# Optimization experiments

Measured on AMD Instinct MI355X. Metric: run time of the kernel, lower is better.

The kernel has to match this reference:

```python
import jax, jax.numpy as jnp
import numpy as np

SCALE = 8.0  # sqrt(d_k), d_k = 64


def setup_inputs() -> dict:
    key = jax.random.key(0)
    kq, kk, kv = jax.random.split(key, 3)
    B, S, D = 16, 2048, 64
    q = jax.random.normal(kq, (B, S, D), dtype=jnp.float32)
    k = jax.random.normal(kk, (B, S, D), dtype=jnp.float32)
    v = jax.random.normal(kv, (B, S, D), dtype=jnp.float32)
    # causal mask: True = masked (future positions), broadcast to batch
    causal = jnp.triu(jnp.ones((S, S), dtype=jnp.bool_), k=1)
    mask = jnp.broadcast_to(causal, (B, S, S))
    return {"q": q, "k": k, "v": v, "mask": mask}


def reference(q, k, v, mask):
    # u = (q @ k^T) / scale  -> [B, S, S]
    u = jnp.einsum("bqd,bkd->bqk", q, k) / SCALE
    u = jnp.where(mask, -jnp.inf, u)
    attn = jax.nn.softmax(u, axis=2)
    output = jnp.einsum("bqk,bkd->bqd", attn, v)
    return (attn, output)
```

## Files before the change

kernel.cpp:

```cpp
#include <hip/hip_runtime.h>
#include <hip/hip_bf16.h>

typedef __attribute__((ext_vector_type(4))) float  f32x4;
typedef __attribute__((ext_vector_type(8))) __bf16 bf16x8;
typedef __attribute__((ext_vector_type(4))) __bf16 bf16x4;

#define S_DIM 2048
#define D_DIM 64
#define A2    0.180336880f
#define TPITCH 68

__device__ __forceinline__ int swz(int r, int c) {
    return r * 64 + (c ^ ((r & 7) << 3));
}

__device__ __forceinline__ void loadK4(const float* Kb, int kt, int tid, f32x4 kr[4]) {
    #pragma unroll
    for (int i = 0; i < 4; ++i)
        kr[i] = *(const f32x4*)(Kb + (size_t)(kt * 64 + (tid >> 4) + i * 16) * D_DIM
                                + (tid & 15) * 4);
}
__device__ __forceinline__ void writeK4(__bf16* buf, int tid, const f32x4 kr[4]) {
    #pragma unroll
    for (int i = 0; i < 4; ++i) {
        bf16x4 h;
        h[0] = (__bf16)kr[i][0]; h[1] = (__bf16)kr[i][1];
        h[2] = (__bf16)kr[i][2]; h[3] = (__bf16)kr[i][3];
        *(bf16x4*)&buf[swz((tid >> 4) + i * 16, (tid & 15) * 4)] = h;
    }
}
__device__ __forceinline__ void loadQfrag(const float* Qb, int w, int c0, int jb, bf16x8 qf[2]) {
    const float* qp = Qb + (w * 16 + c0) * D_DIM + jb * 8;
    #pragma unroll
    for (int h = 0; h < 2; ++h) {
        f32x4 x0 = *(const f32x4*)(qp + h * 32);
        f32x4 x1 = *(const f32x4*)(qp + h * 32 + 4);
        bf16x8 f;
        f[0] = (__bf16)x0[0]; f[1] = (__bf16)x0[1];
        f[2] = (__bf16)x0[2]; f[3] = (__bf16)x0[3];
        f[4] = (__bf16)x1[0]; f[5] = (__bf16)x1[1];
        f[6] = (__bf16)x1[2]; f[7] = (__bf16)x1[3];
        qf[h] = f;
    }
}
__device__ __forceinline__ void mfmaS(const __bf16* bufK, const bf16x8 qf[2],
                                      int c0, int jb, f32x4 sacc[4]) {
    #pragma unroll
    for (int nt = 0; nt < 4; ++nt) sacc[nt] = (f32x4){0.f, 0.f, 0.f, 0.f};
    #pragma unroll
    for (int kk = 0; kk < 2; ++kk) {
        #pragma unroll
        for (int nt = 0; nt < 4; ++nt) {
            bf16x8 kb = *(bf16x8*)&bufK[swz(nt * 16 + c0, kk * 32 + jb * 8)];
            sacc[nt] = __builtin_amdgcn_mfma_f32_16x16x32_bf16(qf[kk], kb, sacc[nt], 0, 0, 0);
        }
    }
}

__global__ __launch_bounds__(256) void tile_pv4_kernel(
    const float* __restrict__ Q, const float* __restrict__ K,
    const float* __restrict__ V, __bf16* __restrict__ obase,
    float* __restrict__ lbase)
{
    __shared__ __attribute__((aligned(16))) __bf16 ldsK[64 * 64];
    __shared__ __attribute__((aligned(16))) __bf16 ldsV[64 * 64];
    __shared__ __attribute__((aligned(16))) __bf16 ldsP[64 * 64];

    const int tid = threadIdx.x, lane = tid & 63, w = tid >> 6;
    const int c0 = lane & 15, jb = lane >> 4;

    const int sid = ((blockIdx.x & 7) << 9) | (blockIdx.x >> 3);
    const int b = sid >> 8, qt = (sid >> 3) & 31, g = sid & 7;
    if (g * 4 > qt) return;
    const int k0 = g * 4, kend = min(k0 + 4, qt + 1);
    const int q0 = qt * 64;
    const size_t slot = (size_t)sid;

    const float* Kb = K + (size_t)b * S_DIM * D_DIM;
    const float* Vb = V + (size_t)b * S_DIM * D_DIM;

    bf16x8 qf[2];
    loadQfrag(Q + ((size_t)b * S_DIM + q0) * D_DIM, w, c0, jb, qf);

    float l2[4] = {0.f, 0.f, 0.f, 0.f};
    f32x4 oacc[4];
    #pragma unroll
    for (int nt = 0; nt < 4; ++nt) oacc[nt] = (f32x4){0.f, 0.f, 0.f, 0.f};

    for (int kt = k0; kt < kend; ++kt) {
        f32x4 kr[4];
        loadK4(Kb, kt, tid, kr);
        writeK4(ldsK, tid, kr);
        {
            float vv[16];
            #pragma unroll
            for (int i = 0; i < 16; ++i)
                vv[i] = Vb[(size_t)(kt * 64 + w * 16 + i) * D_DIM + lane];
            bf16x8 h0, h1;
            #pragma unroll
            for (int j = 0; j < 8; ++j) { h0[j] = (__bf16)vv[j]; h1[j] = (__bf16)vv[8 + j]; }
            *(bf16x8*)&ldsV[swz(lane, w * 16)]     = h0;
            *(bf16x8*)&ldsV[swz(lane, w * 16 + 8)] = h1;
        }
        __syncthreads();

        f32x4 sacc[4];
        mfmaS(ldsK, qf, c0, jb, sacc);
        const bool diag = (kt == qt);
        #pragma unroll
        for (int nt = 0; nt < 4; ++nt) {
            #pragma unroll
            for (int reg = 0; reg < 4; ++reg) {
                const int qr = w * 16 + jb * 4 + reg;
                const int kc = nt * 16 + c0;
                float p = (diag && kc > qr) ? 0.0f : exp2f(sacc[nt][reg] * A2);
                ldsP[swz(qr, kc)] = (__bf16)p;
                l2[reg] += p;
            }
        }
        #pragma unroll
        for (int kk = 0; kk < 2; ++kk) {
            bf16x8 pa = *(bf16x8*)&ldsP[swz(w * 16 + c0, kk * 32 + jb * 8)];
            #pragma unroll
            for (int nt = 0; nt < 4; ++nt) {
                bf16x8 vb = *(bf16x8*)&ldsV[swz(nt * 16 + c0, kk * 32 + jb * 8)];
                oacc[nt] = __builtin_amdgcn_mfma_f32_16x16x32_bf16(pa, vb, oacc[nt], 0, 0, 0);
            }
        }
        __syncthreads();
    }

    #pragma unroll
    for (int reg = 0; reg < 4; ++reg) {
        float l = l2[reg];
        #pragma unroll
        for (int off = 1; off < 16; off <<= 1) l += __shfl_xor(l, off);
        if (c0 == 0) lbase[slot * 64 + w * 16 + jb * 4 + reg] = l;
    }
    #pragma unroll
    for (int nt = 0; nt < 4; ++nt) {
        #pragma unroll
        for (int reg = 0; reg < 4; ++reg) {
            const int qr = w * 16 + jb * 4 + reg;
            obase[slot * 4096 + qr * 64 + nt * 16 + c0] = (__bf16)oacc[nt][reg];
        }
    }
}

__global__ __launch_bounds__(256) void merge4_kernel(
    const __bf16* __restrict__ obase, const float* __restrict__ lbase,
    float* __restrict__ out, float* __restrict__ cef)
{
    const int sid = ((blockIdx.x & 7) << 8) | (blockIdx.x >> 3);
    const int b = sid >> 7, qt = (sid >> 2) & 31, quad = sid & 3;
    const int tid = threadIdx.x;
    const int r  = quad * 16 + (tid >> 4);
    const int c4 = (tid & 15) * 4;
    const int ng = (qt >> 2) + 1;
    const size_t base = (size_t)(b * 32 + qt) * 8;

    float a0 = 0.f, a1 = 0.f, a2 = 0.f, a3 = 0.f, lsum = 0.f;
    for (int g = 0; g < ng; ++g) {
        const __bf16* op = obase + (base + g) * 4096 + r * 64 + c4;
        bf16x4 a = *(const bf16x4*)op;
        a0 += (float)a[0]; a1 += (float)a[1]; a2 += (float)a[2]; a3 += (float)a[3];
        lsum += lbase[(base + g) * 64 + r];
    }
    const float inv = 1.0f / lsum;
    f32x4 o = {a0 * inv, a1 * inv, a2 * inv, a3 * inv};
    *(f32x4*)&out[((size_t)b * S_DIM + qt * 64 + r) * D_DIM + c4] = o;
    if ((tid & 15) == 0) cef[b * S_DIM + qt * 64 + r] = -log2f(lsum);
}

__global__ __launch_bounds__(256) void attn_tile4_kernel(
    const float* __restrict__ Q, const float* __restrict__ K,
    float* __restrict__ attn, const float* __restrict__ cef)
{
    __shared__ __attribute__((aligned(16))) __bf16 ldsK[64 * 64];
    __shared__ __attribute__((aligned(16))) float  ldsT[64 * TPITCH];

    const int tid = threadIdx.x, lane = tid & 63, w = tid >> 6;
    const int c0 = lane & 15, jb = lane >> 4;

    const int sid = ((blockIdx.x & 7) << 9) | (blockIdx.x >> 3);
    const int b = sid >> 8, qt = (sid >> 3) & 31, px = sid & 7;
    const int q0 = qt * 64;
    const int ktbase = px * 4;

    float* rowbase = attn + ((size_t)b * S_DIM + q0) * S_DIM;

    if (ktbase > qt) {
        f32x4 z = {0.f, 0.f, 0.f, 0.f};
        #pragma unroll
        for (int tt = 0; tt < 4; ++tt) {
            float* tileP = rowbase + (ktbase + tt) * 64;
            #pragma unroll
            for (int i = 0; i < 4; ++i) {
                int r  = i * 16 + (tid >> 4);
                int c4 = (tid & 15) * 4;
                *(f32x4*)&tileP[(size_t)r * S_DIM + c4] = z;
            }
        }
        return;
    }

    const float* Kb = K + (size_t)b * S_DIM * D_DIM;
    bf16x8 qf[2];
    loadQfrag(Q + ((size_t)b * S_DIM + q0) * D_DIM, w, c0, jb, qf);
    float ce[4];
    #pragma unroll
    for (int reg = 0; reg < 4; ++reg)
        ce[reg] = cef[b * S_DIM + q0 + w * 16 + jb * 4 + reg];

    for (int tt = 0; tt < 4; ++tt) {
        const int kt = ktbase + tt;
        float* tileP = rowbase + kt * 64;
        if (kt > qt) {
            f32x4 z = {0.f, 0.f, 0.f, 0.f};
            #pragma unroll
            for (int i = 0; i < 4; ++i) {
                int r  = i * 16 + (tid >> 4);
                int c4 = (tid & 15) * 4;
                *(f32x4*)&tileP[(size_t)r * S_DIM + c4] = z;
            }
            continue;
        }
        f32x4 kr[4];
        loadK4(Kb, kt, tid, kr);
        writeK4(ldsK, tid, kr);
        __syncthreads();

        f32x4 sacc[4];
        mfmaS(ldsK, qf, c0, jb, sacc);
        const bool diag = (kt == qt);
        #pragma unroll
        for (int nt = 0; nt < 4; ++nt) {
            #pragma unroll
            for (int reg = 0; reg < 4; ++reg) {
                const int qr = w * 16 + jb * 4 + reg;
                const int kc = nt * 16 + c0;
                float p = (diag && kc > qr) ? 0.0f
                        : exp2f(fmaf(sacc[nt][reg], A2, ce[reg]));
                ldsT[qr * TPITCH + kc] = p;
            }
        }
        __syncthreads();
        #pragma unroll
        for (int i = 0; i < 4; ++i) {
            int r  = i * 16 + (tid >> 4);
            int c4 = (tid & 15) * 4;
            f32x4 x = *(f32x4*)&ldsT[r * TPITCH + c4];
            *(f32x4*)&tileP[(size_t)r * S_DIM + c4] = x;
        }
    }
}

extern "C" void kernel_launch(void* const* d_in, const int* in_sizes, int n_in,
                              void* d_out, int out_size, void* d_ws, size_t ws_size,
                              hipStream_t stream) {
    const float* Q = (const float*)d_in[0];
    const float* K = (const float*)d_in[1];
    const float* V = (const float*)d_in[2];
    float* attn = (float*)d_out;
    float* out  = attn + (size_t)16 * S_DIM * S_DIM;

    __bf16* obase = (__bf16*)d_ws;
    float*  lbase = (float*)((char*)d_ws + (size_t)4096 * 4096 * 2);
    float*  cef   = lbase + (size_t)4096 * 64;

    tile_pv4_kernel <<<dim3(4096), dim3(256), 0, stream>>>(Q, K, V, obase, lbase);
    merge4_kernel   <<<dim3(2048), dim3(256), 0, stream>>>(obase, lbase, out, cef);
    attn_tile4_kernel<<<dim3(4096), dim3(256), 0, stream>>>(Q, K, attn, cef);
}
```

Measured before the change: 95.84 us.

## Compute row sums first, then fuse attention write with PV accumulation

Splits the pipeline into a stats-only pass producing softmax denominators, a small merge, and a fused kernel that writes normalized attention probabilities and accumulates normalized P·V partials in one pass. This removes the separate recomputation of QK for the attention write-out. It adds a lightweight stats pass and kernel launch. It writes attn values from the bf16-rounded P, reducing attn precision.

```diff
diff --git a/kernel.cpp b/kernel.cpp
--- a/kernel.cpp
+++ b/kernel.cpp
@@ -8,7 +8,6 @@
 #define S_DIM 2048
 #define D_DIM 64
 #define A2    0.180336880f
-#define TPITCH 68
 
 __device__ __forceinline__ int swz(int r, int c) {
     return r * 64 + (c ^ ((r & 7) << 3));
@@ -57,14 +56,11 @@
     }
 }
 
-__global__ __launch_bounds__(256) void tile_pv4_kernel(
+__global__ __launch_bounds__(256) void stats4_kernel(
     const float* __restrict__ Q, const float* __restrict__ K,
-    const float* __restrict__ V, __bf16* __restrict__ obase,
-    float* __restrict__ lbase)
+    float* __restrict__ lpart)
 {
     __shared__ __attribute__((aligned(16))) __bf16 ldsK[64 * 64];
-    __shared__ __attribute__((aligned(16))) __bf16 ldsV[64 * 64];
-    __shared__ __attribute__((aligned(16))) __bf16 ldsP[64 * 64];
 
     const int tid = threadIdx.x, lane = tid & 63, w = tid >> 6;
     const int c0 = lane & 15, jb = lane >> 4;
@@ -74,20 +70,113 @@
     if (g * 4 > qt) return;
     const int k0 = g * 4, kend = min(k0 + 4, qt + 1);
     const int q0 = qt * 64;
-    const size_t slot = (size_t)sid;
+
+    const float* Kb = K + (size_t)b * S_DIM * D_DIM;
+    bf16x8 qf[2];
+    loadQfrag(Q + ((size_t)b * S_DIM + q0) * D_DIM, w, c0, jb, qf);
+
+    float l2[4] = {0.f, 0.f, 0.f, 0.f};
+    for (int kt = k0; kt < kend; ++kt) {
+        f32x4 kr[4];
+        loadK4(Kb, kt, tid, kr);
+        writeK4(ldsK, tid, kr);
+        __syncthreads();
+        f32x4 sacc[4];
+        mfmaS(ldsK, qf, c0, jb, sacc);
+        const bool diag = (kt == qt);
+        #pragma unroll
+        for (int nt = 0; nt < 4; ++nt) {
+            #pragma unroll
+            for (int reg = 0; reg < 4; ++reg) {
+                const int qr = w * 16 + jb * 4 + reg;
+                const int kc = nt * 16 + c0;
+                if (!(diag && kc > qr)) l2[reg] += exp2f(sacc[nt][reg] * A2);
+            }
+        }
+        __syncthreads();
+    }
+    #pragma unroll
+    for (int reg = 0; reg < 4; ++reg) {
+        float l = l2[reg];
+        #pragma unroll
+        for (int off = 1; off < 16; off <<= 1) l += __shfl_xor(l, off);
+        if (c0 == 0) lpart[(size_t)sid * 64 + w * 16 + jb * 4 + reg] = l;
+    }
+}
+
+__global__ __launch_bounds__(256) void lmerge_kernel(
+    const float* __restrict__ lpart, float* __restrict__ cef)
+{
+    const int rid = blockIdx.x * 256 + threadIdx.x;
+    const int b = rid >> 11, row = rid & 2047;
+    const int qt = row >> 6, r = row & 63;
+    const int ng = (qt >> 2) + 1;
+    float lsum = 0.f;
+    for (int g = 0; g < ng; ++g)
+        lsum += lpart[(size_t)(b * 256 + qt * 8 + g) * 64 + r];
+    cef[rid] = -log2f(lsum);
+}
+
+__global__ __launch_bounds__(256) void fused4_kernel(
+    const float* __restrict__ Q, const float* __restrict__ K,
+    const float* __restrict__ V, float* __restrict__ attn,
+    __bf16* __restrict__ obase, const float* __restrict__ cef)
+{
+    __shared__ __attribute__((aligned(16))) __bf16 ldsK[64 * 64];
+    __shared__ __attribute__((aligned(16))) __bf16 ldsV[64 * 64];
+    __shared__ __attribute__((aligned(16))) __bf16 ldsP[64 * 64];
+
+    const int tid = threadIdx.x, lane = tid & 63, w = tid >> 6;
+    const int c0 = lane & 15, jb = lane >> 4;
+
+    const int sid = ((blockIdx.x & 7) << 9) | (blockIdx.x >> 3);
+    const int b = sid >> 8, qt = (sid >> 3) & 31, px = sid & 7;
+    const int q0 = qt * 64;
+    const int ktbase = px * 4;
+
+    float* rowbase = attn + ((size_t)b * S_DIM + q0) * S_DIM;
+
+    if (ktbase > qt) {
+        f32x4 z = {0.f, 0.f, 0.f, 0.f};
+        #pragma unroll
+        for (int tt = 0; tt < 4; ++tt) {
+            float* tileP = rowbase + (ktbase + tt) * 64;
+            #pragma unroll
+            for (int i = 0; i < 4; ++i) {
+                int r  = i * 16 + (tid >> 4);
+                int c4 = (tid & 15) * 4;
+                *(f32x4*)&tileP[(size_t)r * S_DIM + c4] = z;
+            }
+        }
+        return;
+    }
 
     const float* Kb = K + (size_t)b * S_DIM * D_DIM;
     const float* Vb = V + (size_t)b * S_DIM * D_DIM;
-
     bf16x8 qf[2];
     loadQfrag(Q + ((size_t)b * S_DIM + q0) * D_DIM, w, c0, jb, qf);
-
-    float l2[4] = {0.f, 0.f, 0.f, 0.f};
+    float ce[4];
+    #pragma unroll
+    for (int reg = 0; reg < 4; ++reg)
+        ce[reg] = cef[b * S_DIM + q0 + w * 16 + jb * 4 + reg];
+
     f32x4 oacc[4];
     #pragma unroll
     for (int nt = 0; nt < 4; ++nt) oacc[nt] = (f32x4){0.f, 0.f, 0.f, 0.f};
 
-    for (int kt = k0; kt < kend; ++kt) {
+    for (int tt = 0; tt < 4; ++tt) {
+        const int kt = ktbase + tt;
+        float* tileP = rowbase + kt * 64;
+        if (kt > qt) {
+            f32x4 z = {0.f, 0.f, 0.f, 0.f};
+            #pragma unroll
+            for (int i = 0; i < 4; ++i) {
+                int r  = i * 16 + (tid >> 4);
+                int c4 = (tid & 15) * 4;
+                *(f32x4*)&tileP[(size_t)r * S_DIM + c4] = z;
+            }
+            continue;
+        }
         f32x4 kr[4];
         loadK4(Kb, kt, tid, kr);
         writeK4(ldsK, tid, kr);
@@ -113,9 +202,9 @@
             for (int reg = 0; reg < 4; ++reg) {
                 const int qr = w * 16 + jb * 4 + reg;
                 const int kc = nt * 16 + c0;
-                float p = (diag && kc > qr) ? 0.0f : exp2f(sacc[nt][reg] * A2);
+                float p = (diag && kc > qr) ? 0.0f
+                        : exp2f(fmaf(sacc[nt][reg], A2, ce[reg]));
                 ldsP[swz(qr, kc)] = (__bf16)p;
-                l2[reg] += p;
             }
         }
         #pragma unroll
@@ -127,29 +216,35 @@
                 oacc[nt] = __builtin_amdgcn_mfma_f32_16x16x32_bf16(pa, vb, oacc[nt], 0, 0, 0);
             }
         }
-        __syncthreads();
-    }
-
-    #pragma unroll
-    for (int reg = 0; reg < 4; ++reg) {
-        float l = l2[reg];
-        #pragma unroll
-        for (int off = 1; off < 16; off <<= 1) l += __shfl_xor(l, off);
-        if (c0 == 0) lbase[slot * 64 + w * 16 + jb * 4 + reg] = l;
-    }
+        #pragma unroll
+        for (int t = 0; t < 2; ++t) {
+            const int row = w * 16 + t * 8 + (lane >> 3);
+            const int c8  = (lane & 7) * 8;
+            bf16x8 pv8 = *(bf16x8*)&ldsP[swz(row, c8)];
+            f32x4 lo, hi;
+            lo[0] = (float)pv8[0]; lo[1] = (float)pv8[1];
+            lo[2] = (float)pv8[2]; lo[3] = (float)pv8[3];
+            hi[0] = (float)pv8[4]; hi[1] = (float)pv8[5];
+            hi[2] = (float)pv8[6]; hi[3] = (float)pv8[7];
+            float* dst = tileP + (size_t)row * S_DIM + c8;
+            *(f32x4*)dst       = lo;
+            *(f32x4*)(dst + 4) = hi;
+        }
+        __syncthreads();
+    }
+
     #pragma unroll
     for (int nt = 0; nt < 4; ++nt) {
         #pragma unroll
         for (int reg = 0; reg < 4; ++reg) {
             const int qr = w * 16 + jb * 4 + reg;
-            obase[slot * 4096 + qr * 64 + nt * 16 + c0] = (__bf16)oacc[nt][reg];
-        }
-    }
-}
-
-__global__ __launch_bounds__(256) void merge4_kernel(
-    const __bf16* __restrict__ obase, const float* __restrict__ lbase,
-    float* __restrict__ out, float* __restrict__ cef)
+            obase[(size_t)sid * 4096 + qr * 64 + nt * 16 + c0] = (__bf16)oacc[nt][reg];
+        }
+    }
+}
+
+__global__ __launch_bounds__(256) void mergeO_kernel(
+    const __bf16* __restrict__ obase, float* __restrict__ out)
 {
     const int sid = ((blockIdx.x & 7) << 8) | (blockIdx.x >> 3);
     const int b = sid >> 7, qt = (sid >> 2) & 31, quad = sid & 3;
@@ -157,102 +252,16 @@
     const int r  = quad * 16 + (tid >> 4);
     const int c4 = (tid & 15) * 4;
     const int ng = (qt >> 2) + 1;
-    const size_t base = (size_t)(b * 32 + qt) * 8;
-
-    float a0 = 0.f, a1 = 0.f, a2 = 0.f, a3 = 0.f, lsum = 0.f;
+    const size_t base = (size_t)(b * 256 + qt * 8);
+
+    float a0 = 0.f, a1 = 0.f, a2 = 0.f, a3 = 0.f;
     for (int g = 0; g < ng; ++g) {
         const __bf16* op = obase + (base + g) * 4096 + r * 64 + c4;
         bf16x4 a = *(const bf16x4*)op;
         a0 += (float)a[0]; a1 += (float)a[1]; a2 += (float)a[2]; a3 += (float)a[3];
-        lsum += lbase[(base + g) * 64 + r];
-    }
-    const float inv = 1.0f / lsum;
-    f32x4 o = {a0 * inv, a1 * inv, a2 * inv, a3 * inv};
+    }
+    f32x4 o = {a0, a1, a2, a3};
     *(f32x4*)&out[((size_t)b * S_DIM + qt * 64 + r) * D_DIM + c4] = o;
-    if ((tid & 15) == 0) cef[b * S_DIM + qt * 64 + r] = -log2f(lsum);
-}
-
-__global__ __launch_bounds__(256) void attn_tile4_kernel(
-    const float* __restrict__ Q, const float* __restrict__ K,
-    float* __restrict__ attn, const float* __restrict__ cef)
-{
-    __shared__ __attribute__((aligned(16))) __bf16 ldsK[64 * 64];
-    __shared__ __attribute__((aligned(16))) float  ldsT[64 * TPITCH];
-
-    const int tid = threadIdx.x, lane = tid & 63, w = tid >> 6;
-    const int c0 = lane & 15, jb = lane >> 4;
-
-    const int sid = ((blockIdx.x & 7) << 9) | (blockIdx.x >> 3);
-    const int b = sid >> 8, qt = (sid >> 3) & 31, px = sid & 7;
-    const int q0 = qt * 64;
-    const int ktbase = px * 4;
-
-    float* rowbase = attn + ((size_t)b * S_DIM + q0) * S_DIM;
-
-    if (ktbase > qt) {
-        f32x4 z = {0.f, 0.f, 0.f, 0.f};
-        #pragma unroll
-        for (int tt = 0; tt < 4; ++tt) {
-            float* tileP = rowbase + (ktbase + tt) * 64;
-            #pragma unroll
-            for (int i = 0; i < 4; ++i) {
-                int r  = i * 16 + (tid >> 4);
-                int c4 = (tid & 15) * 4;
-                *(f32x4*)&tileP[(size_t)r * S_DIM + c4] = z;
-            }
-        }
-        return;
-    }
-
-    const float* Kb = K + (size_t)b * S_DIM * D_DIM;
-    bf16x8 qf[2];
-    loadQfrag(Q + ((size_t)b * S_DIM + q0) * D_DIM, w, c0, jb, qf);
-    float ce[4];
-    #pragma unroll
-    for (int reg = 0; reg < 4; ++reg)
-        ce[reg] = cef[b * S_DIM + q0 + w * 16 + jb * 4 + reg];
-
-    for (int tt = 0; tt < 4; ++tt) {
-        const int kt = ktbase + tt;
-        float* tileP = rowbase + kt * 64;
-        if (kt > qt) {
-            f32x4 z = {0.f, 0.f, 0.f, 0.f};
-            #pragma unroll
-            for (int i = 0; i < 4; ++i) {
-                int r  = i * 16 + (tid >> 4);
-                int c4 = (tid & 15) * 4;
-                *(f32x4*)&tileP[(size_t)r * S_DIM + c4] = z;
-            }
-            continue;
-        }
-        f32x4 kr[4];
-        loadK4(Kb, kt, tid, kr);
-        writeK4(ldsK, tid, kr);
-        __syncthreads();
-
-        f32x4 sacc[4];
-        mfmaS(ldsK, qf, c0, jb, sacc);
-        const bool diag = (kt == qt);
-        #pragma unroll
-        for (int nt = 0; nt < 4; ++nt) {
-            #pragma unroll
-            for (int reg = 0; reg < 4; ++reg) {
-                const int qr = w * 16 + jb * 4 + reg;
-                const int kc = nt * 16 + c0;
-                float p = (diag && kc > qr) ? 0.0f
-                        : exp2f(fmaf(sacc[nt][reg], A2, ce[reg]));
-                ldsT[qr * TPITCH + kc] = p;
-            }
-        }
-        __syncthreads();
-        #pragma unroll
-        for (int i = 0; i < 4; ++i) {
-            int r  = i * 16 + (tid >> 4);
-            int c4 = (tid & 15) * 4;
-            f32x4 x = *(f32x4*)&ldsT[r * TPITCH + c4];
-            *(f32x4*)&tileP[(size_t)r * S_DIM + c4] = x;
-        }
-    }
 }
 
 extern "C" void kernel_launch(void* const* d_in, const int* in_sizes, int n_in,
@@ -265,10 +274,11 @@
     float* out  = attn + (size_t)16 * S_DIM * S_DIM;
 
     __bf16* obase = (__bf16*)d_ws;
-    float*  lbase = (float*)((char*)d_ws + (size_t)4096 * 4096 * 2);
-    float*  cef   = lbase + (size_t)4096 * 64;
-
-    tile_pv4_kernel <<<dim3(4096), dim3(256), 0, stream>>>(Q, K, V, obase, lbase);
-    merge4_kernel   <<<dim3(2048), dim3(256), 0, stream>>>(obase, lbase, out, cef);
-    attn_tile4_kernel<<<dim3(4096), dim3(256), 0, stream>>>(Q, K, attn, cef);
-}
+    float*  lpart = (float*)((char*)d_ws + (size_t)4096 * 4096 * 2);
+    float*  cef   = lpart + (size_t)4096 * 64;
+
+    stats4_kernel<<<dim3(4096), dim3(256), 0, stream>>>(Q, K, lpart);
+    lmerge_kernel<<<dim3(128),  dim3(256), 0, stream>>>(lpart, cef);
+    fused4_kernel<<<dim3(4096), dim3(256), 0, stream>>>(Q, K, V, attn, obase, cef);
+    mergeO_kernel<<<dim3(2048), dim3(256), 0, stream>>>(obase, out);
+}
```

After: 104.5 us. +9.0%, slower.

## Move masked-tile zero fill into PV kernel and compact attention grid

Applied to the files above, without the earlier changes.

Writing zeros for the fully masked upper-triangle attention blocks moves from the final attention kernel into the first PV kernel. There it is interleaved with PV blocks (7 zero blocks per 16 PV blocks), so those stores overlap with compute-bound work instead of sitting alone on the critical path. The attention kernel now launches only the lower-triangle blocks through a compact index mapping, which removes early-exit blocks. The costs are extra index arithmetic and more blocks in the first kernel, and the PV kernel still launches blocks that return early.

```diff
diff --git a/kernel.cpp b/kernel.cpp
--- a/kernel.cpp
+++ b/kernel.cpp
@@ -57,10 +57,10 @@
     }
 }
 
-__global__ __launch_bounds__(256) void tile_pv4_kernel(
+__global__ __launch_bounds__(256) void combo_pv_zero_kernel(
     const float* __restrict__ Q, const float* __restrict__ K,
     const float* __restrict__ V, __bf16* __restrict__ obase,
-    float* __restrict__ lbase)
+    float* __restrict__ lbase, float* __restrict__ attn)
 {
     __shared__ __attribute__((aligned(16))) __bf16 ldsK[64 * 64];
     __shared__ __attribute__((aligned(16))) __bf16 ldsV[64 * 64];
@@ -69,7 +69,33 @@
     const int tid = threadIdx.x, lane = tid & 63, w = tid >> 6;
     const int c0 = lane & 15, jb = lane >> 4;
 
-    const int sid = ((blockIdx.x & 7) << 9) | (blockIdx.x >> 3);
+    const int sgp = blockIdx.x / 23, r23 = blockIdx.x % 23;
+
+    if (r23 >= 16) {
+        const int z0 = sgp * 7 + (r23 - 16);
+        const int z  = (z0 & 7) * 224 + (z0 >> 3);
+        const int b  = z / 112;
+        int u = z % 112, f = 0;
+        for (; f < 8; ++f) { int cnt = 4 * (7 - f); if (u < cnt) break; u -= cnt; }
+        const int m  = u / (7 - f), t = u % (7 - f);
+        const int qt = f * 4 + m, px = f + 1 + t;
+        float* rowbase = attn + ((size_t)b * S_DIM + qt * 64) * S_DIM;
+        f32x4 zv = {0.f, 0.f, 0.f, 0.f};
+        #pragma unroll
+        for (int tt = 0; tt < 4; ++tt) {
+            float* tileP = rowbase + (px * 4 + tt) * 64;
+            #pragma unroll
+            for (int i = 0; i < 4; ++i) {
+                int rr = i * 16 + (tid >> 4);
+                int c4 = (tid & 15) * 4;
+                *(f32x4*)&tileP[(size_t)rr * S_DIM + c4] = zv;
+            }
+        }
+        return;
+    }
+
+    const int p   = sgp * 16 + r23;
+    const int sid = ((p & 7) << 9) | (p >> 3);
     const int b = sid >> 8, qt = (sid >> 3) & 31, g = sid & 7;
     if (g * 4 > qt) return;
     const int k0 = g * 4, kend = min(k0 + 4, qt + 1);
@@ -113,9 +139,9 @@
             for (int reg = 0; reg < 4; ++reg) {
                 const int qr = w * 16 + jb * 4 + reg;
                 const int kc = nt * 16 + c0;
-                float p = (diag && kc > qr) ? 0.0f : exp2f(sacc[nt][reg] * A2);
-                ldsP[swz(qr, kc)] = (__bf16)p;
-                l2[reg] += p;
+                float pp = (diag && kc > qr) ? 0.0f : exp2f(sacc[nt][reg] * A2);
+                ldsP[swz(qr, kc)] = (__bf16)pp;
+                l2[reg] += pp;
             }
         }
         #pragma unroll
@@ -172,7 +198,7 @@
     if ((tid & 15) == 0) cef[b * S_DIM + qt * 64 + r] = -log2f(lsum);
 }
 
-__global__ __launch_bounds__(256) void attn_tile4_kernel(
+__global__ __launch_bounds__(256) void attn_compute_kernel(
     const float* __restrict__ Q, const float* __restrict__ K,
     float* __restrict__ attn, const float* __restrict__ cef)
 {
@@ -182,27 +208,16 @@
     const int tid = threadIdx.x, lane = tid & 63, w = tid >> 6;
     const int c0 = lane & 15, jb = lane >> 4;
 
-    const int sid = ((blockIdx.x & 7) << 9) | (blockIdx.x >> 3);
-    const int b = sid >> 8, qt = (sid >> 3) & 31, px = sid & 7;
+    const int e = (blockIdx.x & 7) * 288 + (blockIdx.x >> 3);
+    const int b = e / 144;
+    int u = e % 144, f = 0;
+    for (; f < 8; ++f) { int cnt = 4 * (f + 1); if (u < cnt) break; u -= cnt; }
+    const int m  = u / (f + 1), px = u % (f + 1);
+    const int qt = f * 4 + m;
     const int q0 = qt * 64;
     const int ktbase = px * 4;
 
     float* rowbase = attn + ((size_t)b * S_DIM + q0) * S_DIM;
-
-    if (ktbase > qt) {
-        f32x4 z = {0.f, 0.f, 0.f, 0.f};
-        #pragma unroll
-        for (int tt = 0; tt < 4; ++tt) {
-            float* tileP = rowbase + (ktbase + tt) * 64;
-            #pragma unroll
-            for (int i = 0; i < 4; ++i) {
-                int r  = i * 16 + (tid >> 4);
-                int c4 = (tid & 15) * 4;
-                *(f32x4*)&tileP[(size_t)r * S_DIM + c4] = z;
-            }
-        }
-        return;
-    }
 
     const float* Kb = K + (size_t)b * S_DIM * D_DIM;
     bf16x8 qf[2];
@@ -219,9 +234,9 @@
             f32x4 z = {0.f, 0.f, 0.f, 0.f};
             #pragma unroll
             for (int i = 0; i < 4; ++i) {
-                int r  = i * 16 + (tid >> 4);
+                int rr = i * 16 + (tid >> 4);
                 int c4 = (tid & 15) * 4;
-                *(f32x4*)&tileP[(size_t)r * S_DIM + c4] = z;
+                *(f32x4*)&tileP[(size_t)rr * S_DIM + c4] = z;
             }
             continue;
         }
@@ -247,10 +262,10 @@
         __syncthreads();
         #pragma unroll
         for (int i = 0; i < 4; ++i) {
-            int r  = i * 16 + (tid >> 4);
+            int rr = i * 16 + (tid >> 4);
             int c4 = (tid & 15) * 4;
-            f32x4 x = *(f32x4*)&ldsT[r * TPITCH + c4];
-            *(f32x4*)&tileP[(size_t)r * S_DIM + c4] = x;
+            f32x4 x = *(f32x4*)&ldsT[rr * TPITCH + c4];
+            *(f32x4*)&tileP[(size_t)rr * S_DIM + c4] = x;
         }
     }
 }
@@ -268,7 +283,7 @@
     float*  lbase = (float*)((char*)d_ws + (size_t)4096 * 4096 * 2);
     float*  cef   = lbase + (size_t)4096 * 64;
 
-    tile_pv4_kernel <<<dim3(4096), dim3(256), 0, stream>>>(Q, K, V, obase, lbase);
-    merge4_kernel   <<<dim3(2048), dim3(256), 0, stream>>>(obase, lbase, out, cef);
-    attn_tile4_kernel<<<dim3(4096), dim3(256), 0, stream>>>(Q, K, attn, cef);
-}
+    combo_pv_zero_kernel<<<dim3(5888), dim3(256), 0, stream>>>(Q, K, V, obase, lbase, attn);
+    merge4_kernel       <<<dim3(2048), dim3(256), 0, stream>>>(obase, lbase, out, cef);
+    attn_compute_kernel <<<dim3(2304), dim3(256), 0, stream>>>(Q, K, attn, cef);
+}
```

Measured after the change: 87.58 us, median of 2. 1.09x faster.
